# Kernel optimization log

Hardware: AMD Instinct MI355X
Metric: run time of the kernel (lower is better)

The kernel has to match this reference:

```python
import jax, jax.numpy as jnp
import numpy as np

BN_EPS = 1e-5
MIN_DIST = 1e-10


def _conv_bn_relu(x, w, b, gamma, beta):
    # pointwise Conv1d (kernel=1) == per-point linear, then BatchNorm1d (training-mode
    # batch stats, biased variance, as torch does for normalization), then ReLU.
    y = jnp.einsum('oc,bcn->bon', w, x) + b[None, :, None]
    mu = y.mean(axis=(0, 2))
    var = y.var(axis=(0, 2))
    yn = (y - mu[None, :, None]) * jax.lax.rsqrt(var + BN_EPS)[None, :, None]
    return jax.nn.relu(yn * gamma[None, :, None] + beta[None, :, None])


def setup_inputs() -> dict:
    key = jax.random.key(0)
    ks = jax.random.split(key, 12)
    B, N1, N2, C1, C2 = 8, 8192, 2048, 128, 256
    in_ch = C1 + C2  # 384
    mlp = [256, 128]
    inp = {
        'xyz1': jax.random.normal(ks[0], (B, N1, 3), jnp.float32),
        'xyz2': jax.random.normal(ks[1], (B, N2, 3), jnp.float32),
        'points1': jax.random.normal(ks[2], (B, C1, N1), jnp.float32),
        'points2': jax.random.normal(ks[3], (B, C2, N2), jnp.float32),
    }
    last = in_ch
    for i, out_ch in enumerate(mlp):
        scale = 1.0 / np.sqrt(last)
        inp[f'w{i}'] = jax.random.uniform(ks[4 + 2 * i], (out_ch, last), jnp.float32, -scale, scale)
        inp[f'b{i}'] = jax.random.uniform(ks[5 + 2 * i], (out_ch,), jnp.float32, -scale, scale)
        inp[f'gamma{i}'] = jnp.ones((out_ch,), jnp.float32)
        inp[f'beta{i}'] = jnp.zeros((out_ch,), jnp.float32)
        last = out_ch
    return inp


def reference(xyz1, xyz2, points1, points2,
              w0, b0, gamma0, beta0, w1, b1, gamma1, beta1):
    # Euclidean distance matrix [B, N1, N2] (torch.cdist, p=2)
    sq = (jnp.sum(xyz1 * xyz1, -1)[:, :, None]
          + jnp.sum(xyz2 * xyz2, -1)[:, None, :]
          - 2.0 * jnp.einsum('bnd,bmd->bnm', xyz1, xyz2))
    dists = jnp.sqrt(jnp.maximum(sq, 0.0))
    # 3 smallest distances + indices (ascending, matching torch.topk largest=False)
    neg_d, knn_idx = jax.lax.top_k(-dists, 3)  # [B, N1, 3]
    knn_d = jnp.maximum(-neg_d, MIN_DIST)
    weights = 1.0 / knn_d
    weights = weights / jnp.sum(weights, axis=2, keepdims=True)  # [B, N1, 3]
    # gather neighbor features: points2 [B, C2, N2] -> [B, C2, N1, 3]
    knn_feats = jnp.take_along_axis(points2[:, :, None, :],
                                    knn_idx[:, None, :, :], axis=3)
    interpolated = jnp.sum(knn_feats * weights[:, None, :, :], axis=3)  # [B, C2, N1]
    new_points = jnp.concatenate([points1, interpolated], axis=1)  # [B, C1+C2, N1]
    new_points = _conv_bn_relu(new_points, w0, b0, gamma0, beta0)
    new_points = _conv_bn_relu(new_points, w1, b1, gamma1, beta1)
    return new_points
```

## Files before the change

### kernel.cpp

```cpp
#include <hip/hip_runtime.h>
#include <cstdint>

using u16 = unsigned short;
typedef short bf16x8 __attribute__((ext_vector_type(8)));
typedef float f32x4 __attribute__((ext_vector_type(4)));

__device__ __forceinline__ float bf2f(u16 h) {
    union { unsigned u; float f; } x;
    x.u = ((unsigned)h) << 16;
    return x.f;
}
__device__ __forceinline__ u16 f2bf(float f) {
    union { float f; unsigned u; } x;
    x.f = f;
    unsigned r = x.u + 0x7fffu + ((x.u >> 16) & 1u);
    return (u16)(r >> 16);
}

__device__ __forceinline__ void gl_lds16(const u16* g, u16* l) {
    __builtin_amdgcn_global_load_lds((const __attribute__((address_space(1))) void*)g,
                                     (__attribute__((address_space(3))) void*)l, 16, 0, 0);
}

#define N1 8192
#define N2 2048
#define C2 256

__device__ __forceinline__ void tr_tile(const float* __restrict__ src,
                                        u16* __restrict__ dst,
                                        int C, int N, int ds, int b, int n0, int c0,
                                        int tid, float (*tile)[33]) {
    int tx = tid & 31, ty = tid >> 5;
    const float* s = src + (long)b * C * N;
#pragma unroll
    for (int i = 0; i < 4; i++) {
        int c = ty + i * 8;
        tile[c][tx] = s[(long)(c0 + c) * N + n0 + tx];
    }
    __syncthreads();
    u16* d = dst + (long)b * N * ds;
#pragma unroll
    for (int i = 0; i < 4; i++) {
        int n = ty + i * 8;
        d[(long)(n0 + n) * ds + c0 + tx] = f2bf(tile[tx][n]);
    }
}

__global__ __launch_bounds__(256) void preproc(const float* __restrict__ w0,
                                               const float* __restrict__ w1,
                                               const float* __restrict__ points1,
                                               const float* __restrict__ points2,
                                               u16* __restrict__ w0b,
                                               u16* __restrict__ w1b,
                                               u16* __restrict__ X,
                                               u16* __restrict__ P2T,
                                               float* __restrict__ stats) {
    __shared__ float tile[32][33];
    int bid = blockIdx.x, tid = threadIdx.x;
    if (bid < 8192) {
        int nb = bid & 255, cb = (bid >> 8) & 3, b = bid >> 10;
        tr_tile(points1, X, 128, 8192, 384, b, nb * 32, cb * 32, tid, tile);
    } else if (bid < 12288) {
        int t = bid - 8192;
        int nb = t & 63, cb = (t >> 6) & 7, b = t >> 9;
        tr_tile(points2, P2T, 256, 2048, 256, b, nb * 32, cb * 32, tid, tile);
    } else if (bid < 12672) {
        int i = (bid - 12288) * 256 + tid;
        w0b[i] = f2bf(w0[i]);
    } else if (bid < 12800) {
        int i = (bid - 12672) * 256 + tid;
        w1b[i] = f2bf(w1[i]);
    } else {
        for (int i = tid; i < 768; i += 256) stats[i] = 0.0f;
    }
}

__global__ __launch_bounds__(512) void knn_interp(const float* __restrict__ xyz1,
                                                  const float* __restrict__ xyz2,
                                                  const u16* __restrict__ P2T,
                                                  u16* __restrict__ X) {
    __shared__ float4 pts[N2 / 2];
    __shared__ float m_d[8][64][3];
    __shared__ int   m_i[8][64][3];
    __shared__ int   s_idx[64][3];
    __shared__ float s_w[64][3];
    int b = blockIdx.y;
    int n0 = blockIdx.x * 64;
    int tid = threadIdx.x;
    int ql = tid & 63;
    int part = tid >> 6;

    int n = n0 + ql;
    float px = xyz1[((long)b * N1 + n) * 3 + 0];
    float py = xyz1[((long)b * N1 + n) * 3 + 1];
    float pz = xyz1[((long)b * N1 + n) * 3 + 2];
    float psq = __fadd_rn(__fadd_rn(__fmul_rn(px, px), __fmul_rn(py, py)), __fmul_rn(pz, pz));

    float b0 = 1e30f, b1 = 1e30f, b2 = 1e30f;
    int i0 = 0, i1 = 0, i2 = 0;

    for (int half = 0; half < 2; half++) {
        for (int j = tid; j < N2 / 2; j += 512) {
            int jg = half * (N2 / 2) + j;
            float x = xyz2[((long)b * N2 + jg) * 3 + 0];
            float y = xyz2[((long)b * N2 + jg) * 3 + 1];
            float z = xyz2[((long)b * N2 + jg) * 3 + 2];
            float nsq = __fadd_rn(__fadd_rn(__fmul_rn(x, x), __fmul_rn(y, y)), __fmul_rn(z, z));
            pts[j] = make_float4(x, y, z, nsq);
        }
        __syncthreads();

        int jbeg = half * (N2 / 2) + part * (N2 / 16);
        const float4* lp = &pts[part * (N2 / 16)];
#pragma unroll 8
        for (int jj = 0; jj < N2 / 16; jj++) {
            int j = jbeg + jj;
            float4 p = lp[jj];
            float dot = __fadd_rn(__fadd_rn(__fmul_rn(px, p.x), __fmul_rn(py, p.y)),
                                  __fmul_rn(pz, p.z));
            float sq = __fsub_rn(__fadd_rn(psq, p.w), __fmul_rn(2.0f, dot));
            if (sq < b2) {
                if (sq < b1) {
                    b2 = b1; i2 = i1;
                    if (sq < b0) { b1 = b0; i1 = i0; b0 = sq; i0 = j; }
                    else         { b1 = sq; i1 = j; }
                } else { b2 = sq; i2 = j; }
            }
        }
        __syncthreads();
    }
    m_d[part][ql][0] = b0; m_d[part][ql][1] = b1; m_d[part][ql][2] = b2;
    m_i[part][ql][0] = i0; m_i[part][ql][1] = i1; m_i[part][ql][2] = i2;
    __syncthreads();

    if (tid < 64) {
        float c0 = 1e30f, c1 = 1e30f, c2 = 1e30f;
        int a0 = 0x7fffffff, a1 = 0x7fffffff, a2 = 0x7fffffff;
#pragma unroll
        for (int pp = 0; pp < 8; pp++) {
#pragma unroll
            for (int k = 0; k < 3; k++) {
                float d = m_d[pp][tid][k];
                int ix = m_i[pp][tid][k];
                if (d < c2 || (d == c2 && ix < a2)) {
                    if (d < c1 || (d == c1 && ix < a1)) {
                        c2 = c1; a2 = a1;
                        if (d < c0 || (d == c0 && ix < a0)) { c1 = c0; a1 = a0; c0 = d; a0 = ix; }
                        else                                { c1 = d; a1 = ix; }
                    } else { c2 = d; a2 = ix; }
                }
            }
        }
        float e0 = sqrtf(fmaxf(c0, 0.0f));
        float e1 = sqrtf(fmaxf(c1, 0.0f));
        float e2 = sqrtf(fmaxf(c2, 0.0f));
        float kd0 = fmaxf(e0, 1e-10f), kd1 = fmaxf(e1, 1e-10f), kd2 = fmaxf(e2, 1e-10f);
        float w0 = __fdiv_rn(1.0f, kd0), w1 = __fdiv_rn(1.0f, kd1), w2 = __fdiv_rn(1.0f, kd2);
        float wsum = __fadd_rn(__fadd_rn(w0, w1), w2);
        s_idx[tid][0] = a0; s_idx[tid][1] = a1; s_idx[tid][2] = a2;
        s_w[tid][0] = __fdiv_rn(w0, wsum);
        s_w[tid][1] = __fdiv_rn(w1, wsum);
        s_w[tid][2] = __fdiv_rn(w2, wsum);
    }
    __syncthreads();

    int l = tid & 63;
    const u16* base = P2T + (long)b * N2 * C2;
    for (int p = part; p < 64; p += 8) {
        int j0 = s_idx[p][0], j1 = s_idx[p][1], j2 = s_idx[p][2];
        float f0 = s_w[p][0], f1 = s_w[p][1], f2 = s_w[p][2];
        ushort4 r0 = *(const ushort4*)&base[(long)j0 * C2 + l * 4];
        ushort4 r1 = *(const ushort4*)&base[(long)j1 * C2 + l * 4];
        ushort4 r2 = *(const ushort4*)&base[(long)j2 * C2 + l * 4];
        ushort4 o;
        o.x = f2bf(__fadd_rn(__fadd_rn(__fmul_rn(bf2f(r0.x), f0), __fmul_rn(bf2f(r1.x), f1)),
                             __fmul_rn(bf2f(r2.x), f2)));
        o.y = f2bf(__fadd_rn(__fadd_rn(__fmul_rn(bf2f(r0.y), f0), __fmul_rn(bf2f(r1.y), f1)),
                             __fmul_rn(bf2f(r2.y), f2)));
        o.z = f2bf(__fadd_rn(__fadd_rn(__fmul_rn(bf2f(r0.z), f0), __fmul_rn(bf2f(r1.z), f1)),
                             __fmul_rn(bf2f(r2.z), f2)));
        o.w = f2bf(__fadd_rn(__fadd_rn(__fmul_rn(bf2f(r0.w), f0), __fmul_rn(bf2f(r1.w), f1)),
                             __fmul_rn(bf2f(r2.w), f2)));
        *(ushort4*)&X[(long)(b * N1 + n0 + p) * 384 + 128 + l * 4] = o;
    }
}

template <int KDIM, bool BN_IN, bool ASYNC>
__global__ __launch_bounds__(256) void gemm_bn(const u16* __restrict__ A,
                                               const u16* __restrict__ Bw,
                                               const float* __restrict__ bias,
                                               const float* __restrict__ g_in_sum,
                                               const float* __restrict__ g_in_ssq,
                                               const float* __restrict__ gamma_in,
                                               const float* __restrict__ beta_in,
                                               u16* __restrict__ Yout, int Ntot,
                                               float* __restrict__ g_out_sum,
                                               float* __restrict__ g_out_ssq) {
    constexpr int LDSZ = ASYNC ? 2 * 128 * 32 : 128 * 40;
    constexpr int SUB = 128 * 32;
    __shared__ __align__(16) u16 Al[LDSZ];
    __shared__ __align__(16) u16 Bl[LDSZ];
    __shared__ float s_stats[256];
    __shared__ float s_scale[BN_IN ? KDIM : 2];
    __shared__ float s_shift[BN_IN ? KDIM : 2];

    int tid = threadIdx.x;
    long s0 = (long)blockIdx.y * 128;
    int o0 = blockIdx.x * 128;

    s_stats[tid] = 0.0f;
    if constexpr (BN_IN) {
        for (int k = tid; k < KDIM; k += 256) {
            float mu = g_in_sum[k] * (1.0f / 65536.0f);
            float var = g_in_ssq[k] * (1.0f / 65536.0f) - mu * mu;
            float rs = rsqrtf(var + 1e-5f);
            float sc = gamma_in[k] * rs;
            s_scale[k] = sc;
            s_shift[k] = beta_in[k] - mu * sc;
        }
    }
    int wid = tid >> 6, lane = tid & 63;
    int wm = wid >> 1, wn = wid & 1;
    int q = lane >> 4, l16 = lane & 15;

    f32x4 acc[4][4];
#pragma unroll
    for (int mi = 0; mi < 4; mi++)
#pragma unroll
        for (int ni = 0; ni < 4; ni++) acc[mi][ni] = (f32x4){0.f, 0.f, 0.f, 0.f};

    int rbase0 = wid * 32;
    int rsub = lane >> 2;
    int colsw = (((lane & 3) ^ (rsub & 3)) << 3);
    const u16* gA0 = A + (s0 + rbase0 + rsub) * KDIM + colsw;
    const u16* gA1 = gA0 + (long)16 * KDIM;
    const u16* gB0 = Bw + (long)(o0 + rbase0 + rsub) * KDIM + colsw;
    const u16* gB1 = gB0 + (long)16 * KDIM;
    u16* lA0 = &Al[rbase0 * 32];
    u16* lA1 = &Al[(rbase0 + 16) * 32];
    u16* lB0 = &Bl[rbase0 * 32];
    u16* lB1 = &Bl[(rbase0 + 16) * 32];
    int qA = ASYNC ? (q ^ (l16 & 3)) : q;

    __syncthreads();

    if constexpr (ASYNC) {
        for (int kt = 0; kt < KDIM; kt += 64) {
#pragma unroll
            for (int sub = 0; sub < 2; sub++) {
                int ko = kt + sub * 32;
                gl_lds16(gA0 + ko, lA0 + sub * SUB);
                gl_lds16(gA1 + ko, lA1 + sub * SUB);
                gl_lds16(gB0 + ko, lB0 + sub * SUB);
                gl_lds16(gB1 + ko, lB1 + sub * SUB);
            }
            __syncthreads();
#pragma unroll
            for (int sub = 0; sub < 2; sub++) {
                bf16x8 af[4], bfr[4];
#pragma unroll
                for (int mi = 0; mi < 4; mi++)
                    af[mi] = *(const bf16x8*)&Al[sub * SUB + (wm * 64 + mi * 16 + l16) * 32 + qA * 8];
#pragma unroll
                for (int ni = 0; ni < 4; ni++)
                    bfr[ni] = *(const bf16x8*)&Bl[sub * SUB + (wn * 64 + ni * 16 + l16) * 32 + qA * 8];
#pragma unroll
                for (int mi = 0; mi < 4; mi++)
#pragma unroll
                    for (int ni = 0; ni < 4; ni++)
                        acc[mi][ni] = __builtin_amdgcn_mfma_f32_16x16x32_bf16(af[mi], bfr[ni],
                                                                              acc[mi][ni], 0, 0, 0);
            }
            __syncthreads();
        }
    } else {
        for (int kt = 0; kt < KDIM; kt += 32) {
#pragma unroll
            for (int cc = 0; cc < 2; cc++) {
                int ci = tid + cc * 256;
                int row = ci >> 2;
                int kc = (ci & 3) << 3;
                union { uint4 u; u16 h[8]; } va;
                va.u = *(const uint4*)(A + (s0 + row) * KDIM + kt + kc);
                if constexpr (BN_IN) {
#pragma unroll
                    for (int j = 0; j < 8; j++) {
                        float f = bf2f(va.h[j]);
                        f = fmaxf(fmaf(f, s_scale[kt + kc + j], s_shift[kt + kc + j]), 0.0f);
                        va.h[j] = f2bf(f);
                    }
                }
                *(uint4*)&Al[row * 40 + kc] = va.u;
                *(uint4*)&Bl[row * 40 + kc] = *(const uint4*)(Bw + (long)(o0 + row) * KDIM + kt + kc);
            }
            __syncthreads();
            bf16x8 af[4], bfr[4];
#pragma unroll
            for (int mi = 0; mi < 4; mi++)
                af[mi] = *(const bf16x8*)&Al[(wm * 64 + mi * 16 + l16) * 40 + qA * 8];
#pragma unroll
            for (int ni = 0; ni < 4; ni++)
                bfr[ni] = *(const bf16x8*)&Bl[(wn * 64 + ni * 16 + l16) * 40 + qA * 8];
#pragma unroll
            for (int mi = 0; mi < 4; mi++)
#pragma unroll
                for (int ni = 0; ni < 4; ni++)
                    acc[mi][ni] = __builtin_amdgcn_mfma_f32_16x16x32_bf16(af[mi], bfr[ni],
                                                                          acc[mi][ni], 0, 0, 0);
            __syncthreads();
        }
    }

#pragma unroll
    for (int ni = 0; ni < 4; ni++) {
        int coll = wn * 64 + ni * 16 + l16;
        int col = o0 + coll;
        float bz = bias[col];
        float s1 = 0.0f, s2 = 0.0f;
#pragma unroll
        for (int mi = 0; mi < 4; mi++) {
#pragma unroll
            for (int r = 0; r < 4; r++) {
                float v = acc[mi][ni][r] + bz;
                s1 += v;
                s2 += v * v;
                long row = s0 + wm * 64 + mi * 16 + q * 4 + r;
                Yout[row * Ntot + col] = f2bf(v);
            }
        }
        s1 += __shfl_xor(s1, 16, 64);
        s1 += __shfl_xor(s1, 32, 64);
        s2 += __shfl_xor(s2, 16, 64);
        s2 += __shfl_xor(s2, 32, 64);
        if (q == 0) {
            atomicAdd(&s_stats[coll], s1);
            atomicAdd(&s_stats[128 + coll], s2);
        }
    }
    __syncthreads();
    if (tid < 128) {
        atomicAdd(&g_out_sum[o0 + tid], s_stats[tid]);
        atomicAdd(&g_out_ssq[o0 + tid], s_stats[128 + tid]);
    }
}

__global__ __launch_bounds__(256) void finalize_k(const u16* __restrict__ Y1,
                                                  const float* __restrict__ g_sum,
                                                  const float* __restrict__ g_ssq,
                                                  const float* __restrict__ gamma,
                                                  const float* __restrict__ beta,
                                                  float* __restrict__ out) {
    __shared__ float s_scale[128], s_shift[128];
    int tid = threadIdx.x;
    if (tid < 128) {
        float mu = g_sum[tid] * (1.0f / 65536.0f);
        float var = g_ssq[tid] * (1.0f / 65536.0f) - mu * mu;
        float rs = rsqrtf(var + 1e-5f);
        float sc = gamma[tid] * rs;
        s_scale[tid] = sc;
        s_shift[tid] = beta[tid] - mu * sc;
    }
    __syncthreads();
    long s = (long)blockIdx.x * 256 + tid;
    int b = (int)(s >> 13);
    int n = (int)(s & 8191);
    const u16* yrow = Y1 + s * 128;
    float* obase = out + (long)b * 128 * 8192 + n;
#pragma unroll
    for (int oc = 0; oc < 128; oc += 8) {
        union { uint4 u; u16 h[8]; } va;
        va.u = *(const uint4*)&yrow[oc];
#pragma unroll
        for (int k = 0; k < 8; k++) {
            int o = oc + k;
            float v = fmaxf(fmaf(bf2f(va.h[k]), s_scale[o], s_shift[o]), 0.0f);
            obase[(long)o * 8192] = v;
        }
    }
}

extern "C" void kernel_launch(void* const* d_in, const int* in_sizes, int n_in,
                              void* d_out, int out_size, void* d_ws, size_t ws_size,
                              hipStream_t stream) {
    const float* xyz1    = (const float*)d_in[0];
    const float* xyz2    = (const float*)d_in[1];
    const float* points1 = (const float*)d_in[2];
    const float* points2 = (const float*)d_in[3];
    const float* w0 = (const float*)d_in[4];
    const float* b0 = (const float*)d_in[5];
    const float* gamma0 = (const float*)d_in[6];
    const float* beta0 = (const float*)d_in[7];
    const float* w1 = (const float*)d_in[8];
    const float* b1 = (const float*)d_in[9];
    const float* gamma1 = (const float*)d_in[10];
    const float* beta1 = (const float*)d_in[11];
    float* out = (float*)d_out;

    char* ws = (char*)d_ws;
    u16* X       = (u16*)(ws + 0);
    u16* P2T     = (u16*)(ws + 50331648);
    u16* w0b     = (u16*)(ws + 58720256);
    u16* w1b     = (u16*)(ws + 58916864);
    u16* Y0      = (u16*)(ws + 58982400);
    u16* Y1b     = (u16*)(ws + 92536832);
    float* stats = (float*)(ws + 109314048);
    if (ws_size < 109317120) return;
    float* gsum0 = stats;
    float* gss0  = stats + 256;
    float* gsum1 = stats + 512;
    float* gss1  = stats + 640;

    preproc<<<12801, 256, 0, stream>>>(w0, w1, points1, points2, w0b, w1b, X, P2T, stats);
    knn_interp<<<dim3(128, 8), 512, 0, stream>>>(xyz1, xyz2, P2T, X);
    gemm_bn<384, false, true><<<dim3(2, 512), 256, 0, stream>>>(
        X, w0b, b0, nullptr, nullptr, nullptr, nullptr, Y0, 256, gsum0, gss0);
    gemm_bn<256, true, false><<<dim3(1, 512), 256, 0, stream>>>(
        Y0, w1b, b1, gsum0, gss0, gamma0, beta0, Y1b, 128, gsum1, gss1);
    finalize_k<<<256, 256, 0, stream>>>(Y1b, gsum1, gss1, gamma1, beta1, out);
}
```

Baseline: 248.9 us.

## Assign one query point per thread in KNN, removing cross-thread top-3 merge

The KNN kernel now gives each thread one query point and has it scan all 2048 reference points, which are loaded once into shared memory, instead of splitting each query across 8 threads and merging partial top-3 lists. The scan loop is double-buffered through registers in chunks of 8, with the distance computations separated from the compare-and-insert chain. This removes the merge phase, the second tile load and extra barriers, but the grid shrinks to 256 blocks of 256 threads. Each thread's serial work grows 8x, and occupancy and latency hiding may suffer on a GPU with many compute units.

```diff
diff --git a/kernel.cpp b/kernel.cpp
--- a/kernel.cpp
+++ b/kernel.cpp
@@ -75,98 +75,93 @@
     }
 }
 
-__global__ __launch_bounds__(512) void knn_interp(const float* __restrict__ xyz1,
+__device__ __forceinline__ void proc8(const float4 (&c)[8], int jb,
+                                      float px, float py, float pz, float psq,
+                                      float& b0, float& b1, float& b2,
+                                      int& i0, int& i1, int& i2) {
+    float sq8[8];
+#pragma unroll
+    for (int u = 0; u < 8; u++) {
+        float dot = __fadd_rn(__fadd_rn(__fmul_rn(px, c[u].x), __fmul_rn(py, c[u].y)),
+                              __fmul_rn(pz, c[u].z));
+        sq8[u] = __fsub_rn(__fadd_rn(psq, c[u].w), __fmul_rn(2.0f, dot));
+    }
+#pragma unroll
+    for (int u = 0; u < 8; u++) {
+        float sq = sq8[u];
+        if (sq < b2) {
+            int j = jb + u;
+            if (sq < b1) {
+                b2 = b1; i2 = i1;
+                if (sq < b0) { b1 = b0; i1 = i0; b0 = sq; i0 = j; }
+                else         { b1 = sq; i1 = j; }
+            } else { b2 = sq; i2 = j; }
+        }
+    }
+}
+
+__global__ __launch_bounds__(256) void knn_interp(const float* __restrict__ xyz1,
                                                   const float* __restrict__ xyz2,
                                                   const u16* __restrict__ P2T,
                                                   u16* __restrict__ X) {
-    __shared__ float4 pts[N2 / 2];
-    __shared__ float m_d[8][64][3];
-    __shared__ int   m_i[8][64][3];
-    __shared__ int   s_idx[64][3];
-    __shared__ float s_w[64][3];
+    __shared__ float4 pts[N2];
+    __shared__ int   s_idx[256][3];
+    __shared__ float s_w[256][3];
     int b = blockIdx.y;
-    int n0 = blockIdx.x * 64;
+    int n0 = blockIdx.x * 256;
     int tid = threadIdx.x;
-    int ql = tid & 63;
-    int part = tid >> 6;
-
-    int n = n0 + ql;
+
+    int n = n0 + tid;
     float px = xyz1[((long)b * N1 + n) * 3 + 0];
     float py = xyz1[((long)b * N1 + n) * 3 + 1];
     float pz = xyz1[((long)b * N1 + n) * 3 + 2];
     float psq = __fadd_rn(__fadd_rn(__fmul_rn(px, px), __fmul_rn(py, py)), __fmul_rn(pz, pz));
 
+    for (int j = tid; j < N2; j += 256) {
+        float x = xyz2[((long)b * N2 + j) * 3 + 0];
+        float y = xyz2[((long)b * N2 + j) * 3 + 1];
+        float z = xyz2[((long)b * N2 + j) * 3 + 2];
+        float nsq = __fadd_rn(__fadd_rn(__fmul_rn(x, x), __fmul_rn(y, y)), __fmul_rn(z, z));
+        pts[j] = make_float4(x, y, z, nsq);
+    }
+    __syncthreads();
+
     float b0 = 1e30f, b1 = 1e30f, b2 = 1e30f;
     int i0 = 0, i1 = 0, i2 = 0;
 
-    for (int half = 0; half < 2; half++) {
-        for (int j = tid; j < N2 / 2; j += 512) {
-            int jg = half * (N2 / 2) + j;
-            float x = xyz2[((long)b * N2 + jg) * 3 + 0];
-            float y = xyz2[((long)b * N2 + jg) * 3 + 1];
-            float z = xyz2[((long)b * N2 + jg) * 3 + 2];
-            float nsq = __fadd_rn(__fadd_rn(__fmul_rn(x, x), __fmul_rn(y, y)), __fmul_rn(z, z));
-            pts[j] = make_float4(x, y, z, nsq);
-        }
-        __syncthreads();
-
-        int jbeg = half * (N2 / 2) + part * (N2 / 16);
-        const float4* lp = &pts[part * (N2 / 16)];
-#pragma unroll 8
-        for (int jj = 0; jj < N2 / 16; jj++) {
-            int j = jbeg + jj;
-            float4 p = lp[jj];
-            float dot = __fadd_rn(__fadd_rn(__fmul_rn(px, p.x), __fmul_rn(py, p.y)),
-                                  __fmul_rn(pz, p.z));
-            float sq = __fsub_rn(__fadd_rn(psq, p.w), __fmul_rn(2.0f, dot));
-            if (sq < b2) {
-                if (sq < b1) {
-                    b2 = b1; i2 = i1;
-                    if (sq < b0) { b1 = b0; i1 = i0; b0 = sq; i0 = j; }
-                    else         { b1 = sq; i1 = j; }
-                } else { b2 = sq; i2 = j; }
-            }
-        }
-        __syncthreads();
-    }
-    m_d[part][ql][0] = b0; m_d[part][ql][1] = b1; m_d[part][ql][2] = b2;
-    m_i[part][ql][0] = i0; m_i[part][ql][1] = i1; m_i[part][ql][2] = i2;
-    __syncthreads();
-
-    if (tid < 64) {
-        float c0 = 1e30f, c1 = 1e30f, c2 = 1e30f;
-        int a0 = 0x7fffffff, a1 = 0x7fffffff, a2 = 0x7fffffff;
-#pragma unroll
-        for (int pp = 0; pp < 8; pp++) {
-#pragma unroll
-            for (int k = 0; k < 3; k++) {
-                float d = m_d[pp][tid][k];
-                int ix = m_i[pp][tid][k];
-                if (d < c2 || (d == c2 && ix < a2)) {
-                    if (d < c1 || (d == c1 && ix < a1)) {
-                        c2 = c1; a2 = a1;
-                        if (d < c0 || (d == c0 && ix < a0)) { c1 = c0; a1 = a0; c0 = d; a0 = ix; }
-                        else                                { c1 = d; a1 = ix; }
-                    } else { c2 = d; a2 = ix; }
-                }
-            }
-        }
-        float e0 = sqrtf(fmaxf(c0, 0.0f));
-        float e1 = sqrtf(fmaxf(c1, 0.0f));
-        float e2 = sqrtf(fmaxf(c2, 0.0f));
+    float4 bA[8], bB[8];
+#pragma unroll
+    for (int u = 0; u < 8; u++) bA[u] = pts[u];
+    for (int j0 = 0; j0 < N2; j0 += 16) {
+        int jb = j0 + 8;
+#pragma unroll
+        for (int u = 0; u < 8; u++) bB[u] = pts[jb + u];
+        proc8(bA, j0, px, py, pz, psq, b0, b1, b2, i0, i1, i2);
+        int ja = (j0 + 16) & (N2 - 1);
+#pragma unroll
+        for (int u = 0; u < 8; u++) bA[u] = pts[ja + u];
+        proc8(bB, jb, px, py, pz, psq, b0, b1, b2, i0, i1, i2);
+    }
+
+    {
+        float e0 = sqrtf(fmaxf(b0, 0.0f));
+        float e1 = sqrtf(fmaxf(b1, 0.0f));
+        float e2 = sqrtf(fmaxf(b2, 0.0f));
         float kd0 = fmaxf(e0, 1e-10f), kd1 = fmaxf(e1, 1e-10f), kd2 = fmaxf(e2, 1e-10f);
         float w0 = __fdiv_rn(1.0f, kd0), w1 = __fdiv_rn(1.0f, kd1), w2 = __fdiv_rn(1.0f, kd2);
         float wsum = __fadd_rn(__fadd_rn(w0, w1), w2);
-        s_idx[tid][0] = a0; s_idx[tid][1] = a1; s_idx[tid][2] = a2;
+        s_idx[tid][0] = i0; s_idx[tid][1] = i1; s_idx[tid][2] = i2;
         s_w[tid][0] = __fdiv_rn(w0, wsum);
         s_w[tid][1] = __fdiv_rn(w1, wsum);
         s_w[tid][2] = __fdiv_rn(w2, wsum);
     }
     __syncthreads();
 
+    int part = tid >> 6;
     int l = tid & 63;
     const u16* base = P2T + (long)b * N2 * C2;
-    for (int p = part; p < 64; p += 8) {
+#pragma unroll 4
+    for (int p = part; p < 256; p += 4) {
         int j0 = s_idx[p][0], j1 = s_idx[p][1], j2 = s_idx[p][2];
         float f0 = s_w[p][0], f1 = s_w[p][1], f2 = s_w[p][2];
         ushort4 r0 = *(const ushort4*)&base[(long)j0 * C2 + l * 4];
@@ -411,7 +406,7 @@
     float* gss1  = stats + 640;
 
     preproc<<<12801, 256, 0, stream>>>(w0, w1, points1, points2, w0b, w1b, X, P2T, stats);
-    knn_interp<<<dim3(128, 8), 512, 0, stream>>>(xyz1, xyz2, P2T, X);
+    knn_interp<<<dim3(32, 8), 256, 0, stream>>>(xyz1, xyz2, P2T, X);
     gemm_bn<384, false, true><<<dim3(2, 512), 256, 0, stream>>>(
         X, w0b, b0, nullptr, nullptr, nullptr, nullptr, Y0, 256, gsum0, gss0);
     gemm_bn<256, true, false><<<dim3(1, 512), 256, 0, stream>>>(
```

Measured after the change: 490.4 us. 1.97x slower.

## Two-pass branchless KNN: med3 threshold pass then thresholded index selection

Applied to the files above, without the earlier changes.

Splits the KNN search into two passes. The first pass computes per-query top-3 distances without indices using branchless fmed3/fmin updates, then reduces them across the 8 partitions to a third-smallest threshold. The second pass recomputes distances and only runs the branchy insertion for candidates at or below that threshold, which is meant to cut wave divergence. All 2048 xyz2 points are now staged in LDS at once (32KB) instead of in two halves. The cost is computing every distance twice, and the larger LDS footprint may lower occupancy.

```diff
diff --git a/kernel.cpp b/kernel.cpp
--- a/kernel.cpp
+++ b/kernel.cpp
@@ -79,9 +79,10 @@
                                                   const float* __restrict__ xyz2,
                                                   const u16* __restrict__ P2T,
                                                   u16* __restrict__ X) {
-    __shared__ float4 pts[N2 / 2];
+    __shared__ float4 pts[N2];
     __shared__ float m_d[8][64][3];
     __shared__ int   m_i[8][64][3];
+    __shared__ float s_thr[64];
     __shared__ int   s_idx[64][3];
     __shared__ float s_w[64][3];
     int b = blockIdx.y;
@@ -96,29 +97,61 @@
     float pz = xyz1[((long)b * N1 + n) * 3 + 2];
     float psq = __fadd_rn(__fadd_rn(__fmul_rn(px, px), __fmul_rn(py, py)), __fmul_rn(pz, pz));
 
+    for (int j = tid; j < N2; j += 512) {
+        float x = xyz2[((long)b * N2 + j) * 3 + 0];
+        float y = xyz2[((long)b * N2 + j) * 3 + 1];
+        float z = xyz2[((long)b * N2 + j) * 3 + 2];
+        float nsq = __fadd_rn(__fadd_rn(__fmul_rn(x, x), __fmul_rn(y, y)), __fmul_rn(z, z));
+        pts[j] = make_float4(x, y, z, nsq);
+    }
+    __syncthreads();
+
+    int jbeg = part * (N2 / 8);
+    const float4* lp = &pts[jbeg];
+
+    float a0 = 1e30f, a1 = 1e30f, a2 = 1e30f;
+#pragma unroll 8
+    for (int jj = 0; jj < N2 / 8; jj++) {
+        float4 p = lp[jj];
+        float dot = __fadd_rn(__fadd_rn(__fmul_rn(px, p.x), __fmul_rn(py, p.y)),
+                              __fmul_rn(pz, p.z));
+        float sq = __fsub_rn(__fadd_rn(psq, p.w), __fmul_rn(2.0f, dot));
+        float n2 = __builtin_amdgcn_fmed3f(a1, a2, sq);
+        float n1 = __builtin_amdgcn_fmed3f(a0, a1, sq);
+        a0 = fminf(a0, sq);
+        a1 = n1; a2 = n2;
+    }
+    m_d[part][ql][0] = a0; m_d[part][ql][1] = a1; m_d[part][ql][2] = a2;
+    __syncthreads();
+
+    if (tid < 64) {
+        float c0 = 1e30f, c1 = 1e30f, c2 = 1e30f;
+#pragma unroll
+        for (int pp = 0; pp < 8; pp++) {
+#pragma unroll
+            for (int k = 0; k < 3; k++) {
+                float d = m_d[pp][tid][k];
+                float n2 = __builtin_amdgcn_fmed3f(c1, c2, d);
+                float n1 = __builtin_amdgcn_fmed3f(c0, c1, d);
+                c0 = fminf(c0, d);
+                c1 = n1; c2 = n2;
+            }
+        }
+        s_thr[tid] = c2;
+    }
+    __syncthreads();
+    float thr = s_thr[ql];
+
     float b0 = 1e30f, b1 = 1e30f, b2 = 1e30f;
-    int i0 = 0, i1 = 0, i2 = 0;
-
-    for (int half = 0; half < 2; half++) {
-        for (int j = tid; j < N2 / 2; j += 512) {
-            int jg = half * (N2 / 2) + j;
-            float x = xyz2[((long)b * N2 + jg) * 3 + 0];
-            float y = xyz2[((long)b * N2 + jg) * 3 + 1];
-            float z = xyz2[((long)b * N2 + jg) * 3 + 2];
-            float nsq = __fadd_rn(__fadd_rn(__fmul_rn(x, x), __fmul_rn(y, y)), __fmul_rn(z, z));
-            pts[j] = make_float4(x, y, z, nsq);
-        }
-        __syncthreads();
-
-        int jbeg = half * (N2 / 2) + part * (N2 / 16);
-        const float4* lp = &pts[part * (N2 / 16)];
+    int i0 = 0x7fffffff, i1 = 0x7fffffff, i2 = 0x7fffffff;
 #pragma unroll 8
-        for (int jj = 0; jj < N2 / 16; jj++) {
+    for (int jj = 0; jj < N2 / 8; jj++) {
+        float4 p = lp[jj];
+        float dot = __fadd_rn(__fadd_rn(__fmul_rn(px, p.x), __fmul_rn(py, p.y)),
+                              __fmul_rn(pz, p.z));
+        float sq = __fsub_rn(__fadd_rn(psq, p.w), __fmul_rn(2.0f, dot));
+        if (sq <= thr) {
             int j = jbeg + jj;
-            float4 p = lp[jj];
-            float dot = __fadd_rn(__fadd_rn(__fmul_rn(px, p.x), __fmul_rn(py, p.y)),
-                                  __fmul_rn(pz, p.z));
-            float sq = __fsub_rn(__fadd_rn(psq, p.w), __fmul_rn(2.0f, dot));
             if (sq < b2) {
                 if (sq < b1) {
                     b2 = b1; i2 = i1;
@@ -127,27 +160,27 @@
                 } else { b2 = sq; i2 = j; }
             }
         }
-        __syncthreads();
-    }
+    }
+    __syncthreads();
     m_d[part][ql][0] = b0; m_d[part][ql][1] = b1; m_d[part][ql][2] = b2;
     m_i[part][ql][0] = i0; m_i[part][ql][1] = i1; m_i[part][ql][2] = i2;
     __syncthreads();
 
     if (tid < 64) {
         float c0 = 1e30f, c1 = 1e30f, c2 = 1e30f;
-        int a0 = 0x7fffffff, a1 = 0x7fffffff, a2 = 0x7fffffff;
+        int a0i = 0x7fffffff, a1i = 0x7fffffff, a2i = 0x7fffffff;
 #pragma unroll
         for (int pp = 0; pp < 8; pp++) {
 #pragma unroll
             for (int k = 0; k < 3; k++) {
                 float d = m_d[pp][tid][k];
                 int ix = m_i[pp][tid][k];
-                if (d < c2 || (d == c2 && ix < a2)) {
-                    if (d < c1 || (d == c1 && ix < a1)) {
-                        c2 = c1; a2 = a1;
-                        if (d < c0 || (d == c0 && ix < a0)) { c1 = c0; a1 = a0; c0 = d; a0 = ix; }
-                        else                                { c1 = d; a1 = ix; }
-                    } else { c2 = d; a2 = ix; }
+                if (d < c2 || (d == c2 && ix < a2i)) {
+                    if (d < c1 || (d == c1 && ix < a1i)) {
+                        c2 = c1; a2i = a1i;
+                        if (d < c0 || (d == c0 && ix < a0i)) { c1 = c0; a1i = a0i; c0 = d; a0i = ix; }
+                        else                                 { c1 = d; a1i = ix; }
+                    } else { c2 = d; a2i = ix; }
                 }
             }
         }
@@ -157,7 +190,7 @@
         float kd0 = fmaxf(e0, 1e-10f), kd1 = fmaxf(e1, 1e-10f), kd2 = fmaxf(e2, 1e-10f);
         float w0 = __fdiv_rn(1.0f, kd0), w1 = __fdiv_rn(1.0f, kd1), w2 = __fdiv_rn(1.0f, kd2);
         float wsum = __fadd_rn(__fadd_rn(w0, w1), w2);
-        s_idx[tid][0] = a0; s_idx[tid][1] = a1; s_idx[tid][2] = a2;
+        s_idx[tid][0] = a0i; s_idx[tid][1] = a1i; s_idx[tid][2] = a2i;
         s_w[tid][0] = __fdiv_rn(w0, wsum);
         s_w[tid][1] = __fdiv_rn(w1, wsum);
         s_w[tid][2] = __fdiv_rn(w2, wsum);
```

After: 271.1 us. 1.09x slower.
